# Optimization experiments

Measured on AMD Instinct MI355X. Metric: run time of the kernel, lower is better.

## Reference

```python
import jax, jax.numpy as jnp
import numpy as np

B, N1, N2 = 8, 16384, 2048
C1, C2 = 128, 256
IN_CH = C1 + C2  # 384
MLP = [256, 128]
BN_EPS = 1e-5


def setup_inputs() -> dict:
    key = jax.random.key(0)
    ks = jax.random.split(key, 12)
    inp = {
        "xyz1": jax.random.normal(ks[0], (B, N1, 3), dtype=jnp.float32),
        "xyz2": jax.random.normal(ks[1], (B, N2, 3), dtype=jnp.float32),
        "points1": jax.random.normal(ks[2], (B, N1, C1), dtype=jnp.float32),
        "points2": jax.random.normal(ks[3], (B, N2, C2), dtype=jnp.float32),
        # pointwise conv1d (kernel=1) weights as [out, in]
        "W1": jax.random.normal(ks[4], (MLP[0], IN_CH), dtype=jnp.float32) * (1.0 / np.sqrt(IN_CH)),
        "b1": jnp.zeros((MLP[0],), dtype=jnp.float32),
        "gamma1": jnp.ones((MLP[0],), dtype=jnp.float32),
        "beta1": jnp.zeros((MLP[0],), dtype=jnp.float32),
        "W2": jax.random.normal(ks[5], (MLP[1], MLP[0]), dtype=jnp.float32) * (1.0 / np.sqrt(MLP[0])),
        "b2": jnp.zeros((MLP[1],), dtype=jnp.float32),
        "gamma2": jnp.ones((MLP[1],), dtype=jnp.float32),
        "beta2": jnp.zeros((MLP[1],), dtype=jnp.float32),
    }
    return inp


def _bn_relu(h, gamma, beta):
    # BatchNorm1d in training mode: batch stats over (B, N) per channel
    mean = jnp.mean(h, axis=(0, 1), keepdims=True)
    var = jnp.mean((h - mean) ** 2, axis=(0, 1), keepdims=True)
    return jax.nn.relu((h - mean) * jax.lax.rsqrt(var + BN_EPS) * gamma + beta)


def reference(xyz1, xyz2, points1, points2, W1, b1, gamma1, beta1, W2, b2, gamma2, beta2):
    # squared pairwise distances [B, N1, N2]
    d = (-2.0 * jnp.einsum("bnc,bmc->bnm", xyz1, xyz2)
         + jnp.sum(xyz1 ** 2, -1)[:, :, None]
         + jnp.sum(xyz2 ** 2, -1)[:, None, :])
    neg_vals, idx = jax.lax.top_k(-d, 3)            # 3 smallest distances
    dists = jnp.maximum(-neg_vals, 1e-10)           # clamp(min=1e-10)
    w = 1.0 / dists                                 # [B, N1, 3]
    w_norm = w / jnp.maximum(jnp.sum(w, axis=2, keepdims=True), 1e-8)
    # gather 3 neighbor features: [B, N1, 3, C2]
    gathered = jax.vmap(lambda p, i: p[i])(points2, idx)
    interp = jnp.einsum("bnk,bnkc->bnc", w_norm, gathered)  # [B, N1, C2]
    x = jnp.concatenate([points1, interp], axis=-1)          # [B, N1, IN_CH]
    # pointwise conv + BN + ReLU stack
    h = jnp.einsum("bnc,oc->bno", x, W1) + b1
    h = _bn_relu(h, gamma1, beta1)
    h = jnp.einsum("bnc,oc->bno", h, W2) + b2
    h = _bn_relu(h, gamma2, beta2)
    return h  # [B, N1, MLP[-1]]
```

## Files before the change

kernel.cpp:

```cpp
#include <hip/hip_runtime.h>
#include <hip/hip_bf16.h>
#include <stdint.h>
#include <stddef.h>

typedef __hip_bfloat16 bf16;
typedef __attribute__((ext_vector_type(8))) short short8;
typedef __attribute__((ext_vector_type(4))) float f32x4;

#define B_SZ   8
#define N1_SZ  16384
#define N2_SZ  2048
#define C1_SZ  128
#define C2_SZ  256
#define IN_CH  384
#define O1_SZ  256
#define O2_SZ  128
#define R_TOT  (B_SZ * N1_SZ)

#define OFF_FLAG   ((size_t)0)
#define OFF_STATS1 ((size_t)256)
#define OFF_SCALE1 ((size_t)2304)
#define OFF_STATS2 ((size_t)4352)
#define OFF_SCALE2 ((size_t)5376)
#define OFF_WIDX   ((size_t)8192)
#define OFF_WW     ((size_t)1581056)
#define OFF_H1     ((size_t)3153920)
#define WS_NEEDED  ((size_t)70262784)


static __device__ __forceinline__ float cvtf(bf16 v) { return __bfloat162float(v); }
static __device__ __forceinline__ float cvtf(float v) { return v; }
static __device__ __forceinline__ bf16  f2b(float v) { return __float2bfloat16(v); }

static __device__ __forceinline__ unsigned umed3(unsigned a, unsigned b, unsigned c) {
  unsigned r;
  asm("v_med3_u32 %0, %1, %2, %3" : "=v"(r) : "v"(a), "v"(b), "v"(c));
  return r;
}

static __device__ __forceinline__ void load8f(const bf16* p, float* f) {
  uint4 v = *(const uint4*)p;
  const bf16* e = (const bf16*)&v;
#pragma unroll
  for (int j = 0; j < 8; ++j) f[j] = cvtf(e[j]);
}
static __device__ __forceinline__ void load8f(const float* p, float* f) {
  float4 a = *(const float4*)p;
  float4 b = *(const float4*)(p + 4);
  f[0] = a.x; f[1] = a.y; f[2] = a.z; f[3] = a.w;
  f[4] = b.x; f[5] = b.y; f[6] = b.z; f[7] = b.w;
}
static __device__ __forceinline__ void load8b(const bf16* p, bf16* o) {
  *(uint4*)o = *(const uint4*)p;
}
static __device__ __forceinline__ void load8b(const float* p, bf16* o) {
  float f[8]; load8f(p, f);
#pragma unroll
  for (int j = 0; j < 8; ++j) o[j] = f2b(f[j]);
}
static __device__ __forceinline__ void stv(bf16* p, float v) { *p = f2b(v); }
static __device__ __forceinline__ void stv(float* p, float v) { *p = v; }
static __device__ __forceinline__ void store8(bf16* p, const bf16* t) { *(uint4*)p = *(const uint4*)t; }
static __device__ __forceinline__ void store8(float* p, const float* t) {
  *(uint4*)p = *(const uint4*)t; *(uint4*)(p + 4) = *(const uint4*)(t + 4);
}

__global__ void k_detect(const uint16_t* __restrict__ probe, int* __restrict__ flag) {
  __shared__ int cnt;
  if (threadIdx.x == 0) cnt = 0;
  __syncthreads();
  unsigned u = probe[threadIdx.x];
  int e = (u >> 7) & 0xFF;
  if (e >= 100 && e <= 141) atomicAdd(&cnt, 1);
  __syncthreads();
  if (threadIdx.x == 0) *flag = (cnt >= 224) ? 1 : 0;
}

template <typename T>
__global__ __launch_bounds__(256) void k_fill2(T* __restrict__ out,
                                               const int* __restrict__ flag, int expect) {
  if (flag && *flag != expect) return;
  size_t e0 = ((size_t)blockIdx.x * 256 + threadIdx.x) * 8;
  T t[8];
#pragma unroll
  for (int j = 0; j < 8; ++j) stv(&t[j], 2.0f);
  store8(out + e0, t);
}

static __device__ __forceinline__ void merge3(double& a0, double& a1, double& a2,
                                              int& x0, int& x1, int& x2, int mask) {
  double b0 = __shfl_xor(a0, mask, 64);
  double b1 = __shfl_xor(a1, mask, 64);
  double b2 = __shfl_xor(a2, mask, 64);
  int y0 = __shfl_xor(x0, mask, 64);
  int y1 = __shfl_xor(x1, mask, 64);
  int y2 = __shfl_xor(x2, mask, 64);
  bool t = (a0 < b0) || (a0 == b0 && x0 < y0);
  double c0 = t ? a0 : b0; int k0 = t ? x0 : y0;
  double A0 = t ? a1 : a0; int X0 = t ? x1 : x0;
  double A1 = t ? a2 : a1; int X1 = t ? x2 : x1;
  double B0 = t ? b0 : b1; int Y0 = t ? y0 : y1;
  double B1 = t ? b1 : b2; int Y1 = t ? y1 : y2;
  t = (A0 < B0) || (A0 == B0 && X0 < Y0);
  double c1 = t ? A0 : B0; int k1 = t ? X0 : Y0;
  double A0b = t ? A1 : A0; int X0b = t ? X1 : X0;
  double B0b = t ? B0 : B1; int Y0b = t ? Y0 : Y1;
  t = (A0b < B0b) || (A0b == B0b && X0b < Y0b);
  double c2 = t ? A0b : B0b; int k2 = t ? X0b : Y0b;
  a0 = c0; a1 = c1; a2 = c2; x0 = k0; x1 = k1; x2 = k2;
}

__global__ __launch_bounds__(512) void k_top3(const void* __restrict__ xyz1v,
                                              const void* __restrict__ xyz2v,
                                              int* __restrict__ widx,
                                              float* __restrict__ ww,
                                              const int* __restrict__ flag) {
  __shared__ float4 sp[N2_SZ];
  int isbf = *flag;
  int b = blockIdx.x >> 7;
  int g = blockIdx.x & 127;
  if (isbf) {
    const bf16* x2 = (const bf16*)xyz2v + (size_t)b * N2_SZ * 3;
    for (int i = threadIdx.x; i < N2_SZ; i += 512) {
      float px = cvtf(x2[i * 3 + 0]);
      float py = cvtf(x2[i * 3 + 1]);
      float pz = cvtf(x2[i * 3 + 2]);
      double dx = (double)px, dy = (double)py, dz = (double)pz;
      sp[i] = make_float4(-2.f * px, -2.f * py, -2.f * pz,
                          (float)(dx * dx + dy * dy + dz * dz));
    }
  } else {
    const float* x2 = (const float*)xyz2v + (size_t)b * N2_SZ * 3;
    for (int i = threadIdx.x; i < N2_SZ; i += 512) {
      float px = x2[i * 3 + 0];
      float py = x2[i * 3 + 1];
      float pz = x2[i * 3 + 2];
      double dx = (double)px, dy = (double)py, dz = (double)pz;
      sp[i] = make_float4(-2.f * px, -2.f * py, -2.f * pz,
                          (float)(dx * dx + dy * dy + dz * dz));
    }
  }
  __syncthreads();
  int qloc = threadIdx.x >> 2;
  int sub  = threadIdx.x & 3;
  int r = b * N1_SZ + g * 128 + qloc;
  float Qxf, Qyf, Qzf;
  if (isbf) {
    const bf16* q = (const bf16*)xyz1v + (size_t)r * 3;
    Qxf = cvtf(q[0]); Qyf = cvtf(q[1]); Qzf = cvtf(q[2]);
  } else {
    const float* q = (const float*)xyz1v + (size_t)r * 3;
    Qxf = q[0]; Qyf = q[1]; Qzf = q[2];
  }

  unsigned m0 = 0xFFFFFFFFu, m1 = 0xFFFFFFFFu, m2 = 0xFFFFFFFFu;
  unsigned m3 = 0xFFFFFFFFu, m4 = 0xFFFFFFFFu;
  const float4* base = sp + sub;
#pragma unroll 4
  for (unsigned i = 0; i < N2_SZ / 4; ++i) {
    float4 p = base[(size_t)i * 4];
    float d = fmaf(p.x, Qxf, fmaf(p.y, Qyf, fmaf(p.z, Qzf, p.w)));
    int bi = __float_as_int(d);
    unsigned u = (unsigned)bi ^ (unsigned)((bi >> 31) | (int)0x80000000);
    unsigned key = (u & 0xFFFFFE00u) | i;
    m4 = umed3(m3, m4, key);
    m3 = umed3(m2, m3, key);
    m2 = umed3(m1, m2, key);
    m1 = umed3(m0, m1, key);
    m0 = m0 < key ? m0 : key;
  }

  double Qx = (double)Qxf, Qy = (double)Qyf, Qz = (double)Qzf;
  double Qn = Qx * Qx + Qy * Qy + Qz * Qz;
  double e0 = 1e300, e1 = 1e300, e2 = 1e300;
  int j0 = 0, j1 = 0, j2 = 0;
  unsigned ms[5] = { m0, m1, m2, m3, m4 };
#pragma unroll
  for (int k = 0; k < 5; ++k) {
    int j = (int)((ms[k] & 511u) << 2) | sub;
    float4 p = sp[j];
    double Px = -0.5 * (double)p.x;
    double Py = -0.5 * (double)p.y;
    double Pz = -0.5 * (double)p.z;
    double pw = Px * Px + Py * Py + Pz * Pz;
    double dot = Qx * Px + Qy * Py + Qz * Pz;
    double d = fma(-2.0, dot, Qn + pw);
    bool l2 = (d < e2) || (d == e2 && j < j2);
    if (l2) {
      bool l1 = (d < e1) || (d == e1 && j < j1);
      if (l1) {
        e2 = e1; j2 = j1;
        bool l0 = (d < e0) || (d == e0 && j < j0);
        if (l0) { e1 = e0; j1 = j0; e0 = d; j0 = j; }
        else    { e1 = d;  j1 = j; }
      } else { e2 = d; j2 = j; }
    }
  }

  merge3(e0, e1, e2, j0, j1, j2, 1);
  merge3(e0, e1, e2, j0, j1, j2, 2);

  if (sub == 0) {
    e0 = fmax(e0, 1e-10); e1 = fmax(e1, 1e-10); e2 = fmax(e2, 1e-10);
    double w0 = 1.0 / e0, w1 = 1.0 / e1, w2 = 1.0 / e2;
    double inv = 1.0 / fmax(w0 + w1 + w2, 1e-8);
    widx[(size_t)r * 3 + 0] = j0; widx[(size_t)r * 3 + 1] = j1; widx[(size_t)r * 3 + 2] = j2;
    ww[(size_t)r * 3 + 0] = (float)(w0 * inv);
    ww[(size_t)r * 3 + 1] = (float)(w1 * inv);
    ww[(size_t)r * 3 + 2] = (float)(w2 * inv);
  }
}

template <typename T>
__global__ __launch_bounds__(512, 4) void k_gemm1(const T* __restrict__ points1,
                                                  const T* __restrict__ points2,
                                                  const int* __restrict__ widx,
                                                  const float* __restrict__ ww,
                                                  const T* __restrict__ W1,
                                                  const T* __restrict__ bias,
                                                  bf16* __restrict__ h1,
                                                  float* __restrict__ part,
                                                  const int* __restrict__ flag, int expect) {
  if (*flag != expect) return;
  constexpr int LDA = 392;
  constexpr int LDT = 40;
  __shared__ bf16 As[64 * LDA];
  __shared__ bf16 Bs[256 * LDT];

  int tid = threadIdx.x;
  int r0 = blockIdx.x * 64;
  int row = tid >> 3;
  int sub = tid & 7;
  int r = r0 + row;
  int bidx = r >> 14;
  int i0 = widx[(size_t)r * 3 + 0];
  int i1 = widx[(size_t)r * 3 + 1];
  int i2 = widx[(size_t)r * 3 + 2];
  float w0 = ww[(size_t)r * 3 + 0];
  float w1 = ww[(size_t)r * 3 + 1];
  float w2 = ww[(size_t)r * 3 + 2];
  const T* p2 = points2 + (size_t)bidx * N2_SZ * C2_SZ;

#pragma unroll
  for (int q = 0; q < 2; ++q) {
    int c = sub * 16 + q * 8;
    bf16 t[8];
    load8b(points1 + (size_t)r * C1_SZ + c, t);
    *(uint4*)&As[row * LDA + c] = *(uint4*)t;
  }
#pragma unroll
  for (int q = 0; q < 4; ++q) {
    int c = sub * 32 + q * 8;
    float f0[8], f1[8], f2[8];
    load8f(p2 + (size_t)i0 * C2_SZ + c, f0);
    load8f(p2 + (size_t)i1 * C2_SZ + c, f1);
    load8f(p2 + (size_t)i2 * C2_SZ + c, f2);
    bf16 t[8];
#pragma unroll
    for (int j = 0; j < 8; ++j)
      t[j] = f2b(w0 * f0[j] + w1 * f1[j] + w2 * f2[j]);
    *(uint4*)&As[row * LDA + C1_SZ + c] = *(uint4*)t;
  }
#pragma unroll
  for (int s = 0; s < 2; ++s) {
    int u = tid + s * 512;
    int orow = u >> 2, okc = (u & 3) * 8;
    bf16 wv0[8];
    load8b(W1 + (size_t)orow * IN_CH + okc, wv0);
    *(uint4*)&Bs[orow * LDT + okc] = *(uint4*)wv0;
  }

  int wave = tid >> 6, lane = tid & 63;
  int quad = lane >> 4, l15 = lane & 15;
  int wy = wave >> 2, wx = wave & 3;

  f32x4 acc[2][4];
#pragma unroll
  for (int tm = 0; tm < 2; ++tm)
#pragma unroll
    for (int tn = 0; tn < 4; ++tn) {
      acc[tm][tn][0] = 0.f; acc[tm][tn][1] = 0.f;
      acc[tm][tn][2] = 0.f; acc[tm][tn][3] = 0.f;
    }

  __syncthreads();

  for (int kk = 0; kk < 12; ++kk) {
    bf16 wv[2][8];
    if (kk < 11) {
#pragma unroll
      for (int s = 0; s < 2; ++s) {
        int u = tid + s * 512;
        int orow = u >> 2, okc = (u & 3) * 8;
        load8b(W1 + (size_t)orow * IN_CH + (kk + 1) * 32 + okc, wv[s]);
      }
    }
    short8 afr[2], bfr[4];
#pragma unroll
    for (int tm = 0; tm < 2; ++tm)
      afr[tm] = *(const short8*)&As[(wy * 32 + tm * 16 + l15) * LDA + kk * 32 + quad * 8];
#pragma unroll
    for (int tn = 0; tn < 4; ++tn)
      bfr[tn] = *(const short8*)&Bs[(wx * 64 + tn * 16 + l15) * LDT + quad * 8];
#pragma unroll
    for (int tm = 0; tm < 2; ++tm)
#pragma unroll
      for (int tn = 0; tn < 4; ++tn)
        acc[tm][tn] = __builtin_amdgcn_mfma_f32_16x16x32_bf16(afr[tm], bfr[tn], acc[tm][tn], 0, 0, 0);
    __syncthreads();
    if (kk < 11) {
#pragma unroll
      for (int s = 0; s < 2; ++s) {
        int u = tid + s * 512;
        int orow = u >> 2, okc = (u & 3) * 8;
        *(uint4*)&Bs[orow * LDT + okc] = *(uint4*)wv[s];
      }
      __syncthreads();
    }
  }

  __syncthreads();
  float* redu = (float*)As;

  float s1[4], s2[4];
#pragma unroll
  for (int tn = 0; tn < 4; ++tn) {
    int col = wx * 64 + tn * 16 + l15;
    float bv = cvtf(bias[col]);
    s1[tn] = 0.f; s2[tn] = 0.f;
#pragma unroll
    for (int tm = 0; tm < 2; ++tm) {
#pragma unroll
      for (int rg = 0; rg < 4; ++rg) {
        int rw = r0 + wy * 32 + tm * 16 + quad * 4 + rg;
        float vv = acc[tm][tn][rg] + bv;
        s1[tn] += vv; s2[tn] += vv * vv;
        h1[(size_t)rw * O1_SZ + col] = f2b(vv);
      }
    }
    s1[tn] += __shfl_xor(s1[tn], 16, 64);
    s1[tn] += __shfl_xor(s1[tn], 32, 64);
    s2[tn] += __shfl_xor(s2[tn], 16, 64);
    s2[tn] += __shfl_xor(s2[tn], 32, 64);
  }
  if (lane < 16) {
#pragma unroll
    for (int tn = 0; tn < 4; ++tn) {
      int col = wx * 64 + tn * 16 + l15;
      redu[(wy * 256 + col) * 2 + 0] = s1[tn];
      redu[(wy * 256 + col) * 2 + 1] = s2[tn];
    }
  }
  __syncthreads();
  {
    float* pb = part + (size_t)blockIdx.x * 512;
    pb[tid] = redu[tid] + redu[512 + tid];
  }
}

template <typename T>
__global__ __launch_bounds__(256) void k_gemm2(const bf16* __restrict__ h1,
                                               const T* __restrict__ W2,
                                               const T* __restrict__ bias,
                                               const float* __restrict__ scale1,
                                               const float* __restrict__ shift1,
                                               T* __restrict__ out,
                                               float* __restrict__ part,
                                               const int* __restrict__ flag, int expect) {
  if (*flag != expect) return;
  constexpr int LDT = 40;
  __shared__ bf16 As[64 * LDT];
  __shared__ bf16 Bs[128 * LDT];
  __shared__ float redu[2][128][2];
  __shared__ float sc_s[O1_SZ], sh_s[O1_SZ];

  int tid = threadIdx.x;
  sc_s[tid] = scale1[tid];
  sh_s[tid] = shift1[tid];

  int r0 = blockIdx.x * 64;
  int arow = tid >> 2;
  int akc  = (tid & 3) * 8;

  int wave = tid >> 6, lane = tid & 63;
  int quad = lane >> 4, l15 = lane & 15;
  int wy = wave >> 1, wx = wave & 1;

  f32x4 acc[2][4];
#pragma unroll
  for (int tm = 0; tm < 2; ++tm)
#pragma unroll
    for (int tn = 0; tn < 4; ++tn) {
      acc[tm][tn][0] = 0.f; acc[tm][tn][1] = 0.f;
      acc[tm][tn][2] = 0.f; acc[tm][tn][3] = 0.f;
    }

  for (int k0 = 0; k0 < O1_SZ; k0 += 32) {
    __syncthreads();
    {
      uint4 v = *(const uint4*)(h1 + (size_t)(r0 + arow) * O1_SZ + k0 + akc);
      const bf16* e = (const bf16*)&v;
      bf16 t[8];
#pragma unroll
      for (int j = 0; j < 8; ++j) {
        float f = cvtf(e[j]);
        f = fmaxf(fmaf(f, sc_s[k0 + akc + j], sh_s[k0 + akc + j]), 0.f);
        t[j] = f2b(f);
      }
      *(uint4*)&As[arow * LDT + akc] = *(uint4*)t;
    }
#pragma unroll
    for (int s = 0; s < 2; ++s) {
      int u = tid + s * 256;
      int orow = u >> 2, okc = (u & 3) * 8;
      bf16 wv[8];
      load8b(W2 + (size_t)orow * O1_SZ + k0 + okc, wv);
      *(uint4*)&Bs[orow * LDT + okc] = *(uint4*)wv;
    }
    __syncthreads();
    short8 afr[2], bfr[4];
#pragma unroll
    for (int tm = 0; tm < 2; ++tm)
      afr[tm] = *(const short8*)&As[(wy * 32 + tm * 16 + l15) * LDT + quad * 8];
#pragma unroll
    for (int tn = 0; tn < 4; ++tn)
      bfr[tn] = *(const short8*)&Bs[(wx * 64 + tn * 16 + l15) * LDT + quad * 8];
#pragma unroll
    for (int tm = 0; tm < 2; ++tm)
#pragma unroll
      for (int tn = 0; tn < 4; ++tn)
        acc[tm][tn] = __builtin_amdgcn_mfma_f32_16x16x32_bf16(afr[tm], bfr[tn], acc[tm][tn], 0, 0, 0);
  }

  float s1[4], s2[4];
#pragma unroll
  for (int tn = 0; tn < 4; ++tn) {
    int col = wx * 64 + tn * 16 + l15;
    float bv = cvtf(bias[col]);
    s1[tn] = 0.f; s2[tn] = 0.f;
#pragma unroll
    for (int tm = 0; tm < 2; ++tm) {
#pragma unroll
      for (int rg = 0; rg < 4; ++rg) {
        int row = r0 + wy * 32 + tm * 16 + quad * 4 + rg;
        float vv = acc[tm][tn][rg] + bv;
        s1[tn] += vv; s2[tn] += vv * vv;
        stv(&out[(size_t)row * O2_SZ + col], vv);
      }
    }
    s1[tn] += __shfl_xor(s1[tn], 16, 64);
    s1[tn] += __shfl_xor(s1[tn], 32, 64);
    s2[tn] += __shfl_xor(s2[tn], 16, 64);
    s2[tn] += __shfl_xor(s2[tn], 32, 64);
  }
  if (lane < 16) {
#pragma unroll
    for (int tn = 0; tn < 4; ++tn) {
      int col = wx * 64 + tn * 16 + l15;
      redu[wy][col][0] = s1[tn];
      redu[wy][col][1] = s2[tn];
    }
  }
  __syncthreads();
  {
    int col = tid & 127;
    int sel = tid >> 7;
    part[(size_t)blockIdx.x * 256 + col * 2 + sel] = redu[0][col][sel] + redu[1][col][sel];
  }
}

__global__ __launch_bounds__(256) void k_reduce(const float* __restrict__ part,
                                                float* __restrict__ stats,
                                                int nblk, int nvals) {
  int v = blockIdx.x;
  float s = 0.f;
  for (int b = threadIdx.x; b < nblk; b += 256)
    s += part[(size_t)b * nvals + v];
  s += __shfl_xor(s, 1, 64);  s += __shfl_xor(s, 2, 64);
  s += __shfl_xor(s, 4, 64);  s += __shfl_xor(s, 8, 64);
  s += __shfl_xor(s, 16, 64); s += __shfl_xor(s, 32, 64);
  __shared__ float red[4];
  if ((threadIdx.x & 63) == 0) red[threadIdx.x >> 6] = s;
  __syncthreads();
  if (threadIdx.x == 0) stats[v] = red[0] + red[1] + red[2] + red[3];
}

__global__ void k_bn_fin(const float* __restrict__ stats, const void* __restrict__ gamma,
                         const void* __restrict__ beta, float* __restrict__ scale,
                         float* __restrict__ shift, int O, float invR,
                         const int* __restrict__ flag) {
  int t = blockIdx.x * blockDim.x + threadIdx.x;
  if (t < O) {
    float gv, bv;
    if (*flag) {
      gv = cvtf(((const bf16*)gamma)[t]); bv = cvtf(((const bf16*)beta)[t]);
    } else {
      gv = ((const float*)gamma)[t];      bv = ((const float*)beta)[t];
    }
    float m = stats[t * 2 + 0] * invR;
    float var = fmaxf(stats[t * 2 + 1] * invR - m * m, 0.f);
    float is = rsqrtf(var + 1e-5f);
    float sc = gv * is;
    scale[t] = sc;
    shift[t] = bv - m * sc;
  }
}

__global__ __launch_bounds__(256) void k_bn_out(void* __restrict__ outv,
                                                const float* __restrict__ scale,
                                                const float* __restrict__ shift,
                                                const int* __restrict__ flag) {
  size_t e0 = ((size_t)blockIdx.x * 256 + threadIdx.x) * 8;
  int c0 = (int)(e0 & (O2_SZ - 1));
  if (*flag) {
    bf16* out = (bf16*)outv;
    float f[8]; load8f(out + e0, f);
    bf16 t[8];
#pragma unroll
    for (int j = 0; j < 8; ++j) {
      float pre = fmaf(f[j], scale[c0 + j], shift[c0 + j]);
      float r = fmaxf(pre, 0.f);
      if (__builtin_isnan(pre)) r = pre;
      stv(&t[j], r);
    }
    store8(out + e0, t);
  } else {
    float* out = (float*)outv;
    float f[8]; load8f(out + e0, f);
    float t[8];
#pragma unroll
    for (int j = 0; j < 8; ++j) {
      float pre = fmaf(f[j], scale[c0 + j], shift[c0 + j]);
      float r = fmaxf(pre, 0.f);
      if (__builtin_isnan(pre)) r = pre;
      t[j] = r;
    }
    store8(out + e0, t);
  }
}

extern "C" void kernel_launch(void* const* d_in, const int* in_sizes, int n_in,
                              void* d_out, int out_size, void* d_ws, size_t ws_size,
                              hipStream_t stream) {
  char* ws = (char*)d_ws;
  int*   flag   = (int*)(ws + OFF_FLAG);
  float* stats1 = (float*)(ws + OFF_STATS1);
  float* scale1 = (float*)(ws + OFF_SCALE1);
  float* shift1 = scale1 + 256;
  float* stats2 = (float*)(ws + OFF_STATS2);
  float* scale2 = (float*)(ws + OFF_SCALE2);
  float* shift2 = scale2 + 128;
  int*   widx   = (int*)(ws + OFF_WIDX);
  float* wwp    = (float*)(ws + OFF_WW);
  bf16*  h1     = (bf16*)(ws + OFF_H1);
  float* part1  = (float*)d_out;
  float* part2  = (float*)(ws + OFF_WIDX);

  const int FILL_GRID = R_TOT * O2_SZ / 2048;

  if (ws_size < WS_NEEDED) {
    if (ws_size >= 256) {
      k_detect<<<1, 256, 0, stream>>>((const uint16_t*)d_in[2], flag);
      k_fill2<bf16><<<FILL_GRID, 256, 0, stream>>>((bf16*)d_out, flag, 1);
      k_fill2<float><<<FILL_GRID, 256, 0, stream>>>((float*)d_out, flag, 0);
    } else {
      k_fill2<bf16><<<FILL_GRID, 256, 0, stream>>>((bf16*)d_out, (const int*)nullptr, 0);
    }
    return;
  }

  k_detect<<<1, 256, 0, stream>>>((const uint16_t*)d_in[2], flag);

  float invR = 1.f / (float)R_TOT;

  k_top3<<<1024, 512, 0, stream>>>(d_in[0], d_in[1], widx, wwp, flag);

  k_gemm1<bf16><<<R_TOT / 64, 512, 0, stream>>>((const bf16*)d_in[2], (const bf16*)d_in[3],
      widx, wwp, (const bf16*)d_in[4], (const bf16*)d_in[5], h1, part1, flag, 1);
  k_gemm1<float><<<R_TOT / 64, 512, 0, stream>>>((const float*)d_in[2], (const float*)d_in[3],
      widx, wwp, (const float*)d_in[4], (const float*)d_in[5], h1, part1, flag, 0);

  k_reduce<<<512, 256, 0, stream>>>(part1, stats1, R_TOT / 64, 512);

  k_bn_fin<<<1, 256, 0, stream>>>(stats1, d_in[6], d_in[7], scale1, shift1, O1_SZ, invR, flag);

  k_gemm2<bf16><<<R_TOT / 64, 256, 0, stream>>>(h1, (const bf16*)d_in[8], (const bf16*)d_in[9],
      scale1, shift1, (bf16*)d_out, part2, flag, 1);
  k_gemm2<float><<<R_TOT / 64, 256, 0, stream>>>(h1, (const float*)d_in[8], (const float*)d_in[9],
      scale1, shift1, (float*)d_out, part2, flag, 0);

  k_reduce<<<256, 256, 0, stream>>>(part2, stats2, R_TOT / 64, 256);

  k_bn_fin<<<1, 128, 0, stream>>>(stats2, d_in[10], d_in[11], scale2, shift2, O2_SZ, invR, flag);

  k_bn_out<<<FILL_GRID, 256, 0, stream>>>(d_out, scale2, shift2, flag);
}
```

Baseline: 392.1 us.

## Split interpolation into its own kernel and accumulate BN1 stats atomically

The inverse-distance gather and interpolation of points2 moves out of the first GEMM kernel into a standalone k_interp kernel. That kernel writes bf16 interpolated features to a scratch buffer aliased on the output, and the GEMM then reads them back with plain vector loads. Per-block BN1 partial sums are replaced by atomic adds into 64 slots, zeroed beforehand, so the following reduction handles far fewer partials. The split adds an extra round trip of the interpolated tensor through global memory plus one redundant zero-valued atomic per thread, in exchange for a simpler, more regular GEMM prologue.

```diff
diff --git a/kernel.cpp b/kernel.cpp
--- a/kernel.cpp
+++ b/kernel.cpp
@@ -74,6 +74,10 @@
   if (e >= 100 && e <= 141) atomicAdd(&cnt, 1);
   __syncthreads();
   if (threadIdx.x == 0) *flag = (cnt >= 224) ? 1 : 0;
+}
+
+__global__ void k_zero(float* __restrict__ s) {
+  s[blockIdx.x * 256 + threadIdx.x] = 0.f;
 }
 
 template <typename T>
@@ -211,27 +215,15 @@
   }
 }
 
-template <typename T>
-__global__ __launch_bounds__(512, 4) void k_gemm1(const T* __restrict__ points1,
-                                                  const T* __restrict__ points2,
-                                                  const int* __restrict__ widx,
-                                                  const float* __restrict__ ww,
-                                                  const T* __restrict__ W1,
-                                                  const T* __restrict__ bias,
-                                                  bf16* __restrict__ h1,
-                                                  float* __restrict__ part,
-                                                  const int* __restrict__ flag, int expect) {
-  if (*flag != expect) return;
-  constexpr int LDA = 392;
-  constexpr int LDT = 40;
-  __shared__ bf16 As[64 * LDA];
-  __shared__ bf16 Bs[256 * LDT];
-
-  int tid = threadIdx.x;
-  int r0 = blockIdx.x * 64;
-  int row = tid >> 3;
-  int sub = tid & 7;
-  int r = r0 + row;
+__global__ __launch_bounds__(256) void k_interp(const void* __restrict__ p2v,
+                                                const int* __restrict__ widx,
+                                                const float* __restrict__ ww,
+                                                bf16* __restrict__ xi,
+                                                const int* __restrict__ flag) {
+  int isbf = *flag;
+  int t = blockIdx.x * 256 + threadIdx.x;
+  int r = t >> 5;
+  int c = (t & 31) << 3;
   int bidx = r >> 14;
   int i0 = widx[(size_t)r * 3 + 0];
   int i1 = widx[(size_t)r * 3 + 1];
@@ -239,7 +231,44 @@
   float w0 = ww[(size_t)r * 3 + 0];
   float w1 = ww[(size_t)r * 3 + 1];
   float w2 = ww[(size_t)r * 3 + 2];
-  const T* p2 = points2 + (size_t)bidx * N2_SZ * C2_SZ;
+  float f0[8], f1[8], f2[8];
+  if (isbf) {
+    const bf16* p2 = (const bf16*)p2v + (size_t)bidx * N2_SZ * C2_SZ;
+    load8f(p2 + (size_t)i0 * C2_SZ + c, f0);
+    load8f(p2 + (size_t)i1 * C2_SZ + c, f1);
+    load8f(p2 + (size_t)i2 * C2_SZ + c, f2);
+  } else {
+    const float* p2 = (const float*)p2v + (size_t)bidx * N2_SZ * C2_SZ;
+    load8f(p2 + (size_t)i0 * C2_SZ + c, f0);
+    load8f(p2 + (size_t)i1 * C2_SZ + c, f1);
+    load8f(p2 + (size_t)i2 * C2_SZ + c, f2);
+  }
+  bf16 o[8];
+#pragma unroll
+  for (int j = 0; j < 8; ++j)
+    o[j] = f2b(w0 * f0[j] + w1 * f1[j] + w2 * f2[j]);
+  *(uint4*)&xi[(size_t)r * C2_SZ + c] = *(uint4*)o;
+}
+
+template <typename T>
+__global__ __launch_bounds__(512, 4) void k_gemm1(const T* __restrict__ points1,
+                                                  const bf16* __restrict__ xi,
+                                                  const T* __restrict__ W1,
+                                                  const T* __restrict__ bias,
+                                                  bf16* __restrict__ h1,
+                                                  float* __restrict__ sbuf,
+                                                  const int* __restrict__ flag, int expect) {
+  if (*flag != expect) return;
+  constexpr int LDA = 392;
+  constexpr int LDT = 40;
+  __shared__ bf16 As[64 * LDA];
+  __shared__ bf16 Bs[256 * LDT];
+
+  int tid = threadIdx.x;
+  int r0 = blockIdx.x * 64;
+  int row = tid >> 3;
+  int sub = tid & 7;
+  int r = r0 + row;
 
 #pragma unroll
   for (int q = 0; q < 2; ++q) {
@@ -251,15 +280,8 @@
 #pragma unroll
   for (int q = 0; q < 4; ++q) {
     int c = sub * 32 + q * 8;
-    float f0[8], f1[8], f2[8];
-    load8f(p2 + (size_t)i0 * C2_SZ + c, f0);
-    load8f(p2 + (size_t)i1 * C2_SZ + c, f1);
-    load8f(p2 + (size_t)i2 * C2_SZ + c, f2);
-    bf16 t[8];
-#pragma unroll
-    for (int j = 0; j < 8; ++j)
-      t[j] = f2b(w0 * f0[j] + w1 * f1[j] + w2 * f2[j]);
-    *(uint4*)&As[row * LDA + C1_SZ + c] = *(uint4*)t;
+    uint4 v = *(const uint4*)&xi[(size_t)r * C2_SZ + c];
+    *(uint4*)&As[row * LDA + C1_SZ + c] = v;
   }
 #pragma unroll
   for (int s = 0; s < 2; ++s) {
@@ -352,10 +374,10 @@
     }
   }
   __syncthreads();
-  {
-    float* pb = part + (size_t)blockIdx.x * 512;
-    pb[tid] = redu[tid] + redu[512 + tid];
-  }
+  atomicAdd(&sbuf[(blockIdx.x & 63) * 512 + tid & 0 ? 0 : (blockIdx.x & 63) * 512 + tid],
+            0.f),
+  sbuf += (size_t)(blockIdx.x & 63) * 512;
+  atomicAdd(&sbuf[tid], redu[tid] + redu[512 + tid]);
 }
 
 template <typename T>
@@ -553,7 +575,8 @@
   int*   widx   = (int*)(ws + OFF_WIDX);
   float* wwp    = (float*)(ws + OFF_WW);
   bf16*  h1     = (bf16*)(ws + OFF_H1);
-  float* part1  = (float*)d_out;
+  bf16*  xi     = (bf16*)d_out;
+  float* sbuf   = (float*)(ws + OFF_WIDX);
   float* part2  = (float*)(ws + OFF_WIDX);
 
   const int FILL_GRID = R_TOT * O2_SZ / 2048;
@@ -575,12 +598,16 @@
 
   k_top3<<<1024, 512, 0, stream>>>(d_in[0], d_in[1], widx, wwp, flag);
 
-  k_gemm1<bf16><<<R_TOT / 64, 512, 0, stream>>>((const bf16*)d_in[2], (const bf16*)d_in[3],
-      widx, wwp, (const bf16*)d_in[4], (const bf16*)d_in[5], h1, part1, flag, 1);
-  k_gemm1<float><<<R_TOT / 64, 512, 0, stream>>>((const float*)d_in[2], (const float*)d_in[3],
-      widx, wwp, (const float*)d_in[4], (const float*)d_in[5], h1, part1, flag, 0);
-
-  k_reduce<<<512, 256, 0, stream>>>(part1, stats1, R_TOT / 64, 512);
+  k_interp<<<R_TOT * 32 / 256, 256, 0, stream>>>(d_in[3], widx, wwp, xi, flag);
+
+  k_zero<<<128, 256, 0, stream>>>(sbuf);
+
+  k_gemm1<bf16><<<R_TOT / 64, 512, 0, stream>>>((const bf16*)d_in[2], xi,
+      (const bf16*)d_in[4], (const bf16*)d_in[5], h1, sbuf, flag, 1);
+  k_gemm1<float><<<R_TOT / 64, 512, 0, stream>>>((const float*)d_in[2], xi,
+      (const float*)d_in[4], (const float*)d_in[5], h1, sbuf, flag, 0);
+
+  k_reduce<<<512, 256, 0, stream>>>(sbuf, stats1, 64, 512);
 
   k_bn_fin<<<1, 256, 0, stream>>>(stats1, d_in[6], d_in[7], scale1, shift1, O1_SZ, invR, flag);
 
```

Result: faster. 376.1 us (-4.1%).
